# Kernel tuning notes

Measured on AMD Instinct MI355X. Metric: run time of the kernel, lower is better.

## Reference

```python
import jax, jax.numpy as jnp
import numpy as np

DIM, HEADS, DH, CHUNK, DEPTH = 1024, 8, 128, 64, 2
BATCH, SEQLEN = 2, 4096
MAX_LR = 0.01
EPS = 1e-6


def _rmsnorm(x, g=None):
    y = x * jax.lax.rsqrt(jnp.mean(x * x, axis=-1, keepdims=True) + EPS)
    return y * g if g is not None else y


def _mem_mlp(ws, x):
    # MemoryMLP: x @ W0, then silu before each subsequent layer
    x = x @ ws[0]
    for w in ws[1:]:
        x = jax.nn.silu(x) @ w
    return x


def _assoc_scan(gates, x):
    # y_t = gates_t * y_{t-1} + x_t along axis 3 (chunk axis)
    g = jnp.broadcast_to(gates, x.shape)
    def op(a, b):
        ga, xa = a
        gb, xb = b
        return ga * gb, gb * xa + xb
    _, y = jax.lax.associative_scan(op, (g, x), axis=3)
    return y


def setup_inputs() -> dict:
    key = jax.random.key(0)
    ks = jax.random.split(key, 12)
    b, n, d, h, dh = BATCH, SEQLEN, DIM, HEADS, DH
    di = h * dh
    lin = lambda k, i, o: jax.random.normal(k, (i, o), jnp.float32) * np.float32(1.0 / np.sqrt(i))
    return {
        "seq": jax.random.normal(ks[0], (b, n, d), jnp.float32),
        "store_norm_g": jnp.ones((d,), jnp.float32),
        "retrieve_norm_g": jnp.ones((d,), jnp.float32),
        "w_kv": lin(ks[1], d, 2 * di),
        "w_q": lin(ks[2], d, di),
        "w_step": lin(ks[3], d, h),
        "w_mom": lin(ks[4], d, h),
        "w_decay": lin(ks[5], d, h),
        "w_gate": lin(ks[6], d, h),
        "w_combine": lin(ks[7], di, d),
        "mh_gamma": jnp.zeros((h, 1, dh), jnp.float32),
        "mem_w0": lin(ks[8], dh, dh),
        "mem_w1": lin(ks[9], dh, dh),
    }


def reference(seq, store_norm_g, retrieve_norm_g, w_kv, w_q, w_step, w_mom,
              w_decay, w_gate, w_combine, mh_gamma, mem_w0, mem_w1):
    b, n, d = seq.shape
    h, dh, c = HEADS, DH, CHUNK
    nc = n // c
    mem_ws = (mem_w0, mem_w1)

    # ---------------- store memories (chunked test-time training) ----------------
    ss = _rmsnorm(seq, store_norm_g)                                    # (b,n,d)
    lr = jax.nn.sigmoid(jnp.einsum('bnd,dh->bhn', ss, w_step)) * MAX_LR  # adaptive step
    lr = lr.reshape(b, h, nc, c)
    cmean = ss.reshape(b, nc, c, d).mean(axis=2)                        # chunk mean-reduce
    mom_gate = jax.nn.sigmoid(jnp.einsum('bnd,dh->bhn', cmean, w_mom))   # (b,h,nc)
    decay = jax.nn.sigmoid(jnp.einsum('bnd,dh->bhn', cmean, w_decay))    # (b,h,nc)

    kv = ss @ w_kv                                                      # (b,n,2*h*dh)
    keys, values = jnp.split(kv, 2, axis=-1)
    split = lambda t: t.reshape(b, n, h, dh).transpose(0, 2, 1, 3).reshape(b, h, nc, c, dh)
    keys, values = split(keys), split(values)

    # per-chunk grad of weighted mse wrt memory MLP weights (vmap(grad), as in torch.func)
    def chunk_loss(ws, k, lrc, v):
        pred = _mem_mlp(ws, k)                                          # (c,dh)
        return jnp.sum(jnp.mean((pred - v) ** 2, axis=-1) * lrc)
    flat = lambda t: t.reshape(b * h * nc, c, dh)
    grads = jax.vmap(jax.grad(chunk_loss), in_axes=(None, 0, 0, 0))(
        mem_ws, flat(keys), lr.reshape(b * h * nc, c), flat(values))
    grads = jnp.stack([g.reshape(b, h, nc, dh, dh) for g in grads])     # (depth,b,h,nc,dh,dh)
    surprise = -grads

    gm = mom_gate[None, :, :, :, None, None]
    gd = (1.0 - decay)[None, :, :, :, None, None]
    momentum = _assoc_scan(gm, surprise)                                # momentum scan over chunks
    updates = _assoc_scan(gd, momentum)                                 # decayed cumulative weight deltas

    # ---------------- retrieve memories ----------------
    sr = _rmsnorm(seq, retrieve_norm_g)
    sr = jnp.pad(sr[:, c - 1:], ((0, 0), (0, c - 1), (0, 0)))           # causal shift by chunk-1
    q = (sr @ w_q).reshape(b, n, h, dh).transpose(0, 2, 1, 3).reshape(b, h, nc, c, dh)

    w0 = mem_w0 + updates[0]                                            # (b,h,nc,dh,dh)
    w1 = mem_w1 + updates[1]
    x = jnp.einsum('bhncd,bhnde->bhnce', q, w0)
    vals = jnp.einsum('bhncd,bhnde->bhnce', jax.nn.silu(x), w1)         # (b,h,nc,c,dh)
    vals = vals.reshape(b, h, n, dh)

    vals = _rmsnorm(vals) * (mh_gamma + 1.0)                            # multihead rmsnorm
    gate = jax.nn.sigmoid(jnp.einsum('bnd,dh->bhn', sr, w_gate))[..., None]
    vals = vals * gate                                                  # retrieve gate (heads>1)
    vals = vals.transpose(0, 2, 1, 3).reshape(b, n, h * dh)             # merge heads
    out = vals @ w_combine                                              # combine heads
    out = jnp.pad(out, ((0, 0), (c - 1, 0), (0, 0)))[:, :n]             # restore alignment
    return out
```

## Files before the change

### kernel.cpp

```cpp
#include <hip/hip_runtime.h>
#include <stdint.h>


#define SEQ 4096
#define NTOK 8192

typedef unsigned short u16;
typedef __attribute__((ext_vector_type(8))) short short8;
typedef __attribute__((ext_vector_type(4))) float f32x4;
typedef __attribute__((ext_vector_type(2))) unsigned int u32x2;

__device__ __forceinline__ u16 f2b(float f) {
  union { float f; uint32_t u; } c; c.f = f;
  uint32_t u = c.u;
  uint32_t r = (u + 0x7fffu + ((u >> 16) & 1u)) >> 16;
  return (u16)r;
}
__device__ __forceinline__ float b2f(u16 h) {
  union { uint32_t u; float f; } c; c.u = ((uint32_t)h) << 16;
  return c.f;
}
__device__ __forceinline__ float sigm(float x) { return 1.f / (1.f + __expf(-x)); }
__device__ __forceinline__ uint32_t pk2(float a, float b) {
  return (uint32_t)f2b(a) | ((uint32_t)f2b(b) << 16);
}
__device__ __forceinline__ void gl16(const void* g, void* l) {
  __builtin_amdgcn_global_load_lds(
      (const __attribute__((address_space(1))) unsigned int*)g,
      (__attribute__((address_space(3))) unsigned int*)l, 16, 0, 0);
}

__device__ __forceinline__ int sidx(int r, int c) {
  return r*128 + ((((c>>3) ^ (r&7))<<3) | (c&7));
}
__device__ __forceinline__ short8 frag_row_lds128(const u16* buf, int row, int ks, int l4) {
  int g = ks*4 + l4;
  return *(const short8*)&buf[row*128 + ((g ^ (row&7))<<3)];
}
__device__ __forceinline__ short8 frag_tile(const u16* t, int row, int ks, int l4) {
  return *(const short8*)&t[row*64 + (((ks*4 + l4) ^ (row&7))<<3)];
}
__device__ __forceinline__ int taddr(int c, int r0) {
  return c*64 + (r0 ^ ((c&7)<<3));
}


__global__ __launch_bounds__(256) void transpose_bf16(
    const float* __restrict__ src, u16* __restrict__ dst, int R, int C)
{
  __shared__ u16 tile[64*66];
  int tiles_x = C >> 6;
  int tx = blockIdx.x % tiles_x, ty = blockIdx.x / tiles_x;
  int c0 = tx*64, r0 = ty*64;
#pragma unroll
  for (int it=0; it<16; ++it) {
    int idx = it*256 + threadIdx.x;
    int rr = idx>>6, cc = idx&63;
    tile[cc*66 + rr] = f2b(src[(size_t)(r0+rr)*C + c0+cc]);
  }
  __syncthreads();
#pragma unroll
  for (int it=0; it<16; ++it) {
    int idx = it*256 + threadIdx.x;
    int rr = idx>>6, cc = idx&63;
    dst[(size_t)(c0+rr)*R + r0+cc] = tile[rr*66 + cc];
  }
}

__global__ __launch_bounds__(256) void smallprep(
    const float* __restrict__ w0, const float* __restrict__ w1,
    u16* __restrict__ w0Ts, u16* __restrict__ w1Ts, u16* __restrict__ w1bs)
{
  int id = blockIdx.x*256 + threadIdx.x;
  int i = id>>7, j = id&127;
  float a = w0[id], b = w1[id];
  w0Ts[sidx(j,i)] = f2b(a);
  w1Ts[sidx(j,i)] = f2b(b);
  w1bs[sidx(i,j)] = f2b(b);
}

__global__ __launch_bounds__(256) void proj_prep(
    const float* __restrict__ wstep, const float* __restrict__ wgatew,
    u16* __restrict__ Bt16)
{
  int id = blockIdx.x*256 + threadIdx.x;
  int n = id>>10, k = id&1023;
  float v = (n < 8) ? wstep[k*8 + n] : wgatew[k*8 + (n-8)];
  Bt16[id] = f2b(v);
}


__global__ __launch_bounds__(256) void norms_only(
    const float* __restrict__ seq, const float* __restrict__ gs,
    const float* __restrict__ gr, u16* __restrict__ ss, u16* __restrict__ sr)
{
  int w = threadIdx.x>>6, lane = threadIdx.x&63;
  int t = blockIdx.x*4 + w;
  const float* row = seq + (size_t)t*1024;
  f32x4 x[4];
  float ssq = 0.f;
#pragma unroll
  for (int j=0;j<4;++j) {
    x[j] = *(const f32x4*)&row[j*256 + lane*4];
    ssq += x[j][0]*x[j][0] + x[j][1]*x[j][1] + x[j][2]*x[j][2] + x[j][3]*x[j][3];
  }
  for (int m=32;m;m>>=1) ssq += __shfl_xor(ssq, m);
  float inv = rsqrtf(ssq*(1.f/1024.f) + 1e-6f);
#pragma unroll
  for (int j=0;j<4;++j) {
    int d = j*256 + lane*4;
    f32x4 g4 = *(const f32x4*)&gs[d];
    f32x4 r4 = *(const f32x4*)&gr[d];
    u32x2 ps, pr;
    ps[0] = pk2(x[j][0]*inv*g4[0], x[j][1]*inv*g4[1]);
    ps[1] = pk2(x[j][2]*inv*g4[2], x[j][3]*inv*g4[3]);
    pr[0] = pk2(x[j][0]*inv*r4[0], x[j][1]*inv*r4[1]);
    pr[1] = pk2(x[j][2]*inv*r4[2], x[j][3]*inv*r4[3]);
    *(u32x2*)&ss[(size_t)t*1024 + d] = ps;
    *(u32x2*)&sr[(size_t)t*1024 + d] = pr;
  }
}


__global__ __launch_bounds__(64) void proj_kernel(
    const u16* __restrict__ ss, const u16* __restrict__ sr,
    const u16* __restrict__ Bt16, float* __restrict__ lr,
    float* __restrict__ gate)
{
  int lane = threadIdx.x;
  int l15 = lane&15, l4 = lane>>4;
  size_t t0 = (size_t)blockIdx.x*16;
  f32x4 acc1 = {}, acc2 = {};
#pragma unroll 8
  for (int ks=0; ks<32; ++ks) {
    int kof = ks*32 + l4*8;
    short8 bf = *(const short8*)&Bt16[l15*1024 + kof];
    short8 as = *(const short8*)&ss[(t0+l15)*1024 + kof];
    short8 ar = *(const short8*)&sr[(t0+l15)*1024 + kof];
    acc1 = __builtin_amdgcn_mfma_f32_16x16x32_bf16(as, bf, acc1, 0,0,0);
    acc2 = __builtin_amdgcn_mfma_f32_16x16x32_bf16(ar, bf, acc2, 0,0,0);
  }
  int col = l15;
#pragma unroll
  for (int j=0;j<4;++j) {
    int t = (int)t0 + l4*4 + j;
    int b = t>>12, pos = t&4095;
    if (col < 8) lr[((size_t)(b*8+col))*4096 + pos] = sigm(acc1[j])*0.01f;
    else gate[((size_t)(b*8+(col-8)))*4096 + pos] = sigm(acc2[j]);
  }
}


__global__ __launch_bounds__(256) void chunkgates_kernel(
    const u16* __restrict__ ss, const float* __restrict__ wmom,
    const float* __restrict__ wdec, float* __restrict__ mg,
    float* __restrict__ d1m)
{
  int bc = blockIdx.x; int b = bc>>6, ch = bc&63;
  size_t t0 = (size_t)(b*4096 + ch*64)*1024;
  int tid = threadIdx.x;
  float cm[4]; cm[0]=cm[1]=cm[2]=cm[3]=0.f;
  for (int tok=0; tok<64; ++tok) {
#pragma unroll
    for (int i=0;i<4;++i)
      cm[i] += b2f(ss[t0 + (size_t)tok*1024 + i*256 + tid]);
  }
  float pm[8], pd[8];
#pragma unroll
  for (int h=0;h<8;++h){ pm[h]=0.f; pd[h]=0.f; }
#pragma unroll
  for (int i=0;i<4;++i) {
    float v = cm[i]*(1.f/64.f);
    int d = i*256+tid;
#pragma unroll
    for (int h=0;h<8;++h){ pm[h]+=v*wmom[d*8+h]; pd[h]+=v*wdec[d*8+h]; }
  }
#pragma unroll
  for (int h=0;h<8;++h)
    for (int m=32;m;m>>=1){ pm[h] += __shfl_xor(pm[h],m); pd[h] += __shfl_xor(pd[h],m); }
  __shared__ float r2[4][16];
  int wv = tid>>6;
  if ((tid&63)==0) {
#pragma unroll
    for (int h=0;h<8;++h){ r2[wv][h]=pm[h]; r2[wv][8+h]=pd[h]; }
  }
  __syncthreads();
  if (tid < 16) {
    float s = r2[0][tid]+r2[1][tid]+r2[2][tid]+r2[3][tid];
    if (tid<8) mg[(b*8+tid)*64 + ch] = sigm(s);
    else d1m[(b*8+(tid-8))*64 + ch] = 1.f - sigm(s);
  }
}


__global__ __launch_bounds__(512, 4) void gemm_bt(
    const u16* __restrict__ A, const u16* __restrict__ Bt,
    void* __restrict__ C, int M, int N, int K, int out_f32,
    u16* __restrict__ kvT)
{
  __shared__ __align__(16) u16 As[2][128*64];
  __shared__ __align__(16) u16 Bs[2][128*64];
  int tid = threadIdx.x;
  int w = tid>>6, lane = tid&63;
  int wr = w>>2, wc = w&3;
  int l15 = lane&15, l4 = lane>>4;
  int rl = lane>>3;
  int cg = (lane&7) ^ rl;
  int nwg = gridDim.x*gridDim.y;
  int wg  = blockIdx.y*gridDim.x + blockIdx.x;
  int cpx = nwg >> 3;
  int swz = (wg & 7)*cpx + (wg >> 3);
  int bx = swz % gridDim.x, by = swz / gridDim.x;
  int brow = by*128, bcol = bx*128;
  f32x4 acc[4][2] = {};

  auto STAGE = [&](int buf, int kt) {
#pragma unroll
    for (int i=0;i<2;++i) {
      int row = w*16 + i*8;
      gl16(&A [(size_t)(brow+row+rl)*K + kt + cg*8], &As[buf][row*64]);
      gl16(&Bt[(size_t)(bcol+row+rl)*K + kt + cg*8], &Bs[buf][row*64]);
    }
  };

  int nk = K >> 6;
  STAGE(0, 0);
  asm volatile("s_waitcnt vmcnt(0)");
  __syncthreads();
  for (int t=0; t<nk; ++t) {
    int cur = t & 1;
    if (t+1 < nk) STAGE(cur^1, (t+1)*64);
#pragma unroll
    for (int ks=0; ks<2; ++ks) {
      short8 af[4], bf[2];
#pragma unroll
      for (int m=0;m<4;++m) {
        int row = wr*64 + m*16 + l15;
        int g = ks*4 + l4;
        af[m] = *(const short8*)&As[cur][row*64 + ((g ^ (row&7))<<3)];
      }
#pragma unroll
      for (int n=0;n<2;++n) {
        int row = wc*32 + n*16 + l15;
        int g = ks*4 + l4;
        bf[n] = *(const short8*)&Bs[cur][row*64 + ((g ^ (row&7))<<3)];
      }
#pragma unroll
      for (int m=0;m<4;++m)
#pragma unroll
        for (int n=0;n<2;++n)
          acc[m][n] = __builtin_amdgcn_mfma_f32_16x16x32_bf16(af[m], bf[n], acc[m][n], 0,0,0);
    }
    asm volatile("s_waitcnt vmcnt(0)");
    __syncthreads();
  }
#pragma unroll
  for (int m=0;m<4;++m) {
#pragma unroll
    for (int n=0;n<2;++n) {
      int col = bcol + wc*32 + n*16 + l15;
#pragma unroll
      for (int j=0;j<4;++j) {
        int row = brow + wr*64 + m*16 + l4*4 + j;
        if (out_f32) ((float*)C)[(size_t)row*N + col] = acc[m][n][j];
        else ((u16*)C)[(size_t)row*N + col] = f2b(acc[m][n][j]);
      }
    }
  }
  if (kvT) {
#pragma unroll
    for (int m=0;m<4;++m) {
#pragma unroll
      for (int n=0;n<2;++n) {
        int col = bcol + wc*32 + n*16 + l15;
        if (col < 1024) {
          int row0 = brow + wr*64 + m*16 + l4*4;
          int d = col & 127;
          int chunk = ((row0>>12)*8 + (col>>7))*64 + ((row0&4095)>>6);
          int rr = row0 & 63;
          u32x2 p; p[0] = pk2(acc[m][n][0], acc[m][n][1]);
                   p[1] = pk2(acc[m][n][2], acc[m][n][3]);
          *(u32x2*)&kvT[(size_t)chunk*8192 + taddr(d, rr)] = p;
        }
      }
    }
  }
}


__global__ __launch_bounds__(512) void mlp_fwd(
    const u16* __restrict__ kvout, const float* __restrict__ lr,
    const u16* __restrict__ w0Ts, const u16* __restrict__ w1Ts,
    const u16* __restrict__ w1bs,
    u16* __restrict__ aTg, u16* __restrict__ dpTg, u16* __restrict__ dxTg)
{
  __shared__ __align__(16) u16 W0L[16384];
  __shared__ __align__(16) u16 W1L[16384];
  __shared__ __align__(16) u16 WBL[16384];
  __shared__ __align__(16) u16 abuf[16384];
  int tid = threadIdx.x;
  int w = tid>>6, lane = tid&63;
  int l15 = lane&15, l4 = lane>>4;
#pragma unroll
  for (int it=0; it<4; ++it) {
    int wb = it*512 + w*64;
    gl16((const short8*)w0Ts + wb + lane, (short8*)W0L + wb);
    gl16((const short8*)w1Ts + wb + lane, (short8*)W1L + wb);
    gl16((const short8*)w1bs + wb + lane, (short8*)WBL + wb);
  }
  __syncthreads();
  u16* ab = abuf + w*2048;
  int r0 = l4*4;
  int q = w&3, half = w>>2;
  int rb = q*16;
#pragma unroll
  for (int it2=0; it2<2; ++it2) {
    int cidx = blockIdx.x*4 + it2*2 + half;
    int bh = cidx>>6, ch = cidx&63;
    int b = bh>>3, hh = bh&7;
    size_t t0 = (size_t)(b*4096 + ch*64 + rb);
    size_t tout = (size_t)cidx*8192;
    f32x4 lrv = *(const f32x4*)&lr[(size_t)bh*4096 + ch*64 + rb + r0];

    f32x4 x1[8] = {};
#pragma unroll
    for (int ks=0; ks<4; ++ks) {
      short8 af = *(const short8*)&kvout[(t0 + l15)*2048 + hh*128 + ks*32 + l4*8];
#pragma unroll
      for (int n=0;n<8;++n) {
        short8 bf = frag_row_lds128(W0L, n*16+l15, ks, l4);
        x1[n] = __builtin_amdgcn_mfma_f32_16x16x32_bf16(af, bf, x1[n], 0,0,0);
      }
    }
#pragma unroll
    for (int n=0;n<8;++n) {
      int c = n*16 + l15;
      float av[4];
#pragma unroll
      for (int j=0;j<4;++j){ float xv = x1[n][j]; av[j] = xv*sigm(xv); }
      ab[sidx(r0+0,c)] = f2b(av[0]);
      ab[sidx(r0+1,c)] = f2b(av[1]);
      ab[sidx(r0+2,c)] = f2b(av[2]);
      ab[sidx(r0+3,c)] = f2b(av[3]);
      u32x2 p; p[0] = pk2(av[0],av[1]); p[1] = pk2(av[2],av[3]);
      *(u32x2*)&aTg[tout + taddr(c, rb + r0)] = p;
    }
    f32x4 pr[8] = {};
#pragma unroll
    for (int ks=0; ks<4; ++ks) {
      short8 af = frag_row_lds128(ab, l15, ks, l4);
#pragma unroll
      for (int n=0;n<8;++n) {
        short8 bf = frag_row_lds128(W1L, n*16+l15, ks, l4);
        pr[n] = __builtin_amdgcn_mfma_f32_16x16x32_bf16(af, bf, pr[n], 0,0,0);
      }
    }
#pragma unroll
    for (int n=0;n<8;++n) {
      int c = n*16 + l15;
      float dv[4];
#pragma unroll
      for (int j=0;j<4;++j) {
        float vv = b2f(kvout[(t0+r0+j)*2048 + 1024 + hh*128 + c]);
        dv[j] = 0.015625f * lrv[j] * (pr[n][j] - vv);
      }
      ab[sidx(r0+0,c)] = f2b(dv[0]);
      ab[sidx(r0+1,c)] = f2b(dv[1]);
      ab[sidx(r0+2,c)] = f2b(dv[2]);
      ab[sidx(r0+3,c)] = f2b(dv[3]);
      u32x2 p; p[0] = pk2(dv[0],dv[1]); p[1] = pk2(dv[2],dv[3]);
      *(u32x2*)&dpTg[tout + taddr(c, rb + r0)] = p;
    }
    f32x4 da[8] = {};
#pragma unroll
    for (int ks=0; ks<4; ++ks) {
      short8 af = frag_row_lds128(ab, l15, ks, l4);
#pragma unroll
      for (int n=0;n<8;++n) {
        short8 bf = frag_row_lds128(WBL, n*16+l15, ks, l4);
        da[n] = __builtin_amdgcn_mfma_f32_16x16x32_bf16(af, bf, da[n], 0,0,0);
      }
    }
#pragma unroll
    for (int n=0;n<8;++n) {
      int c = n*16 + l15;
      float d[4];
#pragma unroll
      for (int j=0;j<4;++j) {
        float xv = x1[n][j];
        float sg = sigm(xv);
        d[j] = da[n][j]*(sg*(1.f + xv*(1.f - sg)));
      }
      u32x2 p; p[0] = pk2(d[0],d[1]); p[1] = pk2(d[2],d[3]);
      *(u32x2*)&dxTg[tout + taddr(c, rb + r0)] = p;
    }
  }
}


__global__ __launch_bounds__(256) void grad_op(
    const u16* __restrict__ dpT, const u16* __restrict__ aT,
    const u16* __restrict__ dxT, const u16* __restrict__ kT,
    u16* __restrict__ S)
{
  __shared__ __align__(16) u16 lds[16384];
  int bid = blockIdx.x;
  int op = bid >> 10;
  int sub = bid & 1023, bh = sub>>6, ch = sub&63;
  size_t tin = (size_t)sub*8192;
  const u16* Ain = op ? (dxT + tin) : (dpT + tin);
  const u16* Bin = op ? (kT  + tin) : (aT  + tin);
  int tid = threadIdx.x;
  int w = tid>>6, lane = tid&63;
  int l15 = lane&15, l4 = lane>>4;

#pragma unroll
  for (int it=0; it<4; ++it) {
    int wb = it*256 + w*64;
    gl16((const short8*)Ain + wb + lane, (short8*)lds + wb);
    gl16((const short8*)Bin + wb + lane, (short8*)(lds+8192) + wb);
  }
  __syncthreads();

  f32x4 g[2][8] = {};
#pragma unroll
  for (int ks=0; ks<2; ++ks) {
    short8 af[2];
#pragma unroll
    for (int mi=0; mi<2; ++mi)
      af[mi] = frag_tile(lds, w*32 + mi*16 + l15, ks, l4);
#pragma unroll
    for (int n=0;n<8;++n) {
      short8 bf = frag_tile(lds+8192, n*16 + l15, ks, l4);
#pragma unroll
      for (int mi=0;mi<2;++mi)
        g[mi][n] = __builtin_amdgcn_mfma_f32_16x16x32_bf16(af[mi], bf, g[mi][n], 0,0,0);
    }
  }
  __syncthreads();

#pragma unroll
  for (int mi=0;mi<2;++mi)
#pragma unroll
    for (int n=0;n<8;++n)
#pragma unroll
      for (int j=0;j<4;++j) {
        int m = w*32 + mi*16 + l4*4 + j, c = n*16 + l15;
        lds[sidx(m,c)] = f2b(-g[mi][n][j]);
      }
  __syncthreads();

  u16* Sout = S + ((size_t)((op ? bh : 16+bh))*64 + ch)*16384;
#pragma unroll
  for (int it=0; it<8; ++it)
    ((short8*)Sout)[it*256+tid] = ((const short8*)lds)[it*256+tid];
}


__global__ __launch_bounds__(256) void scan_kernel(
    u16* __restrict__ S, const float* __restrict__ mg, const float* __restrict__ d1m,
    const u16* __restrict__ w0Ts, const u16* __restrict__ w1Ts)
{
  int bidx = blockIdx.x;
  int eblk = bidx & 31;
  int mbh = bidx >> 5;
  int bh = mbh & 15;
  int e = (eblk*256 + threadIdx.x)*2;
  uint32_t* base = (uint32_t*)(S + (size_t)mbh*64*16384 + e);
  const u16* wsrc = (mbh < 16) ? w0Ts : w1Ts;
  uint32_t wp = *(const uint32_t*)&wsrc[e];
  float wv0 = b2f((u16)(wp & 0xffffu)), wv1 = b2f((u16)(wp >> 16));
  const float* g1 = mg + bh*64;
  const float* g2 = d1m + bh*64;
  float mom0=0.f, upd0=0.f, mom1=0.f, upd1=0.f;
  for (int c2=0; c2<64; ++c2) {
    uint32_t s2 = base[(size_t)c2*8192];
    float s0 = b2f((u16)(s2 & 0xffffu)), s1 = b2f((u16)(s2 >> 16));
    float gg1 = g1[c2], gg2 = g2[c2];
    mom0 = gg1*mom0 + s0; upd0 = gg2*upd0 + mom0;
    mom1 = gg1*mom1 + s1; upd1 = gg2*upd1 + mom1;
    base[(size_t)c2*8192] = pk2(wv0 + upd0, wv1 + upd1);
  }
}


__global__ __launch_bounds__(256) void retrieve_kernel(
    const u16* __restrict__ qn, const u16* __restrict__ W,
    const float* __restrict__ gamma, const float* __restrict__ gate,
    u16* __restrict__ vals)
{
  __shared__ __align__(16) u16 W0s[16384];
  __shared__ __align__(16) u16 W1s[16384];
  __shared__ __align__(16) u16 QA[8192];
  int bid = blockIdx.x;
  int bh = bid>>6, ch = bid&63;
  int b = bh>>3, h = bh&7;
  int tid = threadIdx.x;
  int w = tid>>6, lane = tid&63;
  int l15 = lane&15, l4 = lane>>4;
  const u16* W0g = W + ((size_t)bh*64 + ch)*16384;
  const u16* W1g = W + ((size_t)(16+bh)*64 + ch)*16384;
#pragma unroll
  for (int it=0; it<8; ++it) {
    int wb = it*256 + w*64;
    gl16((const short8*)W0g + wb + lane, (short8*)W0s + wb);
    gl16((const short8*)W1g + wb + lane, (short8*)W1s + wb);
  }
  u16* qa = QA + w*2048;
#pragma unroll
  for (int it=0; it<4; ++it) {
    int task = it*64 + lane;
    int rloc = task>>4, g = task&15;
    int posn = ch*64 + w*16 + rloc + 63;
    short8 v;
    if (posn < 4096) v = *(const short8*)&qn[((size_t)(b*4096+posn))*1024 + h*128 + g*8];
    else {
#pragma unroll
      for (int i=0;i<8;++i) v[i]=0;
    }
    *(short8*)&qa[rloc*128 + ((g ^ (rloc&7))<<3)] = v;
  }
  __syncthreads();
  f32x4 xx[8] = {};
#pragma unroll
  for (int ks=0; ks<4; ++ks) {
    short8 af = frag_row_lds128(qa, l15, ks, l4);
#pragma unroll
    for (int n=0;n<8;++n) {
      short8 bf = frag_row_lds128(W0s, n*16+l15, ks, l4);
      xx[n] = __builtin_amdgcn_mfma_f32_16x16x32_bf16(af, bf, xx[n], 0,0,0);
    }
  }
  int r0 = l4*4;
#pragma unroll
  for (int n=0;n<8;++n) {
    int c = n*16 + l15;
#pragma unroll
    for (int j=0;j<4;++j) {
      float xv = xx[n][j];
      qa[sidx(r0+j,c)] = f2b(xv * sigm(xv));
    }
  }
  f32x4 vv[8] = {};
#pragma unroll
  for (int ks=0; ks<4; ++ks) {
    short8 af = frag_row_lds128(qa, l15, ks, l4);
#pragma unroll
    for (int n=0;n<8;++n) {
      short8 bf = frag_row_lds128(W1s, n*16+l15, ks, l4);
      vv[n] = __builtin_amdgcn_mfma_f32_16x16x32_bf16(af, bf, vv[n], 0,0,0);
    }
  }
#pragma unroll
  for (int j=0;j<4;++j) {
    float ssq = 0.f;
#pragma unroll
    for (int n=0;n<8;++n) ssq += vv[n][j]*vv[n][j];
    ssq += __shfl_xor(ssq,1); ssq += __shfl_xor(ssq,2);
    ssq += __shfl_xor(ssq,4); ssq += __shfl_xor(ssq,8);
    float rms = rsqrtf(ssq*(1.f/128.f) + 1e-6f);
    int posn = ch*64 + w*16 + r0 + j + 63;
    if (posn < 4096) {
      float gt = gate[(size_t)bh*4096 + posn];
      size_t orow = ((size_t)(b*4096+posn))*1024 + h*128;
#pragma unroll
      for (int n=0;n<8;++n) {
        int c = n*16 + l15;
        vals[orow + c] = f2b(vv[n][j]*rms*(1.f + gamma[h*128+c])*gt);
      }
    }
  }
}

extern "C" void kernel_launch(void* const* d_in, const int* in_sizes, int n_in,
                              void* d_out, int out_size, void* d_ws, size_t ws_size,
                              hipStream_t stream) {
  const float* seq    = (const float*)d_in[0];
  const float* gstore = (const float*)d_in[1];
  const float* gret   = (const float*)d_in[2];
  const float* wkv    = (const float*)d_in[3];
  const float* wq     = (const float*)d_in[4];
  const float* wstep  = (const float*)d_in[5];
  const float* wmom   = (const float*)d_in[6];
  const float* wdec   = (const float*)d_in[7];
  const float* wgatew = (const float*)d_in[8];
  const float* wcomb  = (const float*)d_in[9];
  const float* gamma  = (const float*)d_in[10];
  const float* w0f    = (const float*)d_in[11];
  const float* w1f    = (const float*)d_in[12];
  float* out = (float*)d_out;
  (void)in_sizes; (void)n_in; (void)out_size; (void)ws_size;

  char* p = (char*)d_ws;
  size_t off = 0;
  auto alloc = [&](size_t bytes) -> void* {
    void* r = p + off; off += (bytes + 255) & ~(size_t)255; return r;
  };
  u16* wkvT   = (u16*)alloc((size_t)2048*1024*2);
  u16* wqT    = (u16*)alloc((size_t)1024*1024*2);
  u16* wcombT = (u16*)alloc((size_t)1024*1024*2);
  u16* w0Ts   = (u16*)alloc(16384*2);
  u16* w1Ts   = (u16*)alloc(16384*2);
  u16* w1bs   = (u16*)alloc(16384*2);
  u16* Bt16   = (u16*)alloc(16384*2);
  u16* ss     = (u16*)alloc((size_t)NTOK*1024*2);
  u16* sr     = (u16*)alloc((size_t)NTOK*1024*2);
  u16* kvout  = (u16*)alloc((size_t)NTOK*2048*2);
  u16* qn     = (u16*)alloc((size_t)NTOK*1024*2);
  u16* vals   = (u16*)alloc((size_t)NTOK*1024*2);
  float* lr   = (float*)alloc((size_t)16*4096*4);
  float* gate = (float*)alloc((size_t)16*4096*4);
  float* mg   = (float*)alloc(1024*4);
  float* d1m  = (float*)alloc(1024*4);
  u16* S      = (u16*)alloc((size_t)32*64*16384*2);
  u16* kTg    = (u16*)alloc((size_t)1024*8192*2);
  u16* aTg    = (u16*)alloc((size_t)1024*8192*2);
  u16* dpTg   = (u16*)alloc((size_t)1024*8192*2);
  u16* dxTg   = (u16*)alloc((size_t)1024*8192*2);

  transpose_bf16<<<dim3(512),dim3(256),0,stream>>>(wkv, wkvT, 1024, 2048);
  transpose_bf16<<<dim3(256),dim3(256),0,stream>>>(wq, wqT, 1024, 1024);
  transpose_bf16<<<dim3(256),dim3(256),0,stream>>>(wcomb, wcombT, 1024, 1024);
  smallprep<<<dim3(64),dim3(256),0,stream>>>(w0f, w1f, w0Ts, w1Ts, w1bs);
  proj_prep<<<dim3(64),dim3(256),0,stream>>>(wstep, wgatew, Bt16);
  norms_only<<<dim3(2048),dim3(256),0,stream>>>(seq, gstore, gret, ss, sr);
  proj_kernel<<<dim3(512),dim3(64),0,stream>>>(ss, sr, Bt16, lr, gate);
  chunkgates_kernel<<<dim3(128),dim3(256),0,stream>>>(ss, wmom, wdec, mg, d1m);
  gemm_bt<<<dim3(16,64),dim3(512),0,stream>>>(ss, wkvT, kvout, 8192, 2048, 1024, 0, kTg);
  gemm_bt<<<dim3(8,64),dim3(512),0,stream>>>(sr, wqT, qn, 8192, 1024, 1024, 0, nullptr);
  mlp_fwd<<<dim3(256),dim3(512),0,stream>>>(kvout, lr, w0Ts, w1Ts, w1bs, aTg, dpTg, dxTg);
  grad_op<<<dim3(2048),dim3(256),0,stream>>>(dpTg, aTg, dxTg, kTg, S);
  scan_kernel<<<dim3(1024),dim3(256),0,stream>>>(S, mg, d1m, w0Ts, w1Ts);
  hipMemsetAsync(vals, 0, 63*1024*2, stream);
  hipMemsetAsync(vals + (size_t)4096*1024, 0, 63*1024*2, stream);
  retrieve_kernel<<<dim3(1024),dim3(256),0,stream>>>(qn, S, gamma, gate, vals);
  gemm_bt<<<dim3(8,64),dim3(512),0,stream>>>(vals, wcombT, out, 8192, 1024, 1024, 1, nullptr);
}
```

Measured before the change: 238.3 us.

## Fuse per-chunk weight-gradient outer products into the MLP forward kernel

```diff
diff --git a/kernel.cpp b/kernel.cpp
--- a/kernel.cpp
+++ b/kernel.cpp
@@ -37,11 +37,15 @@
   int g = ks*4 + l4;
   return *(const short8*)&buf[row*128 + ((g ^ (row&7))<<3)];
 }
-__device__ __forceinline__ short8 frag_tile(const u16* t, int row, int ks, int l4) {
-  return *(const short8*)&t[row*64 + (((ks*4 + l4) ^ (row&7))<<3)];
-}
-__device__ __forceinline__ int taddr(int c, int r0) {
-  return c*64 + (r0 ^ ((c&7)<<3));
+__device__ __forceinline__ int swzOP(int dim, int k) {
+  return dim*32 + ((((k>>3) ^ (dim&3)))<<3) + (k&7);
+}
+__device__ __forceinline__ void opw4(u16* tb, int dim, int k0, uint32_t p0, uint32_t p1) {
+  u32x2 v; v[0] = p0; v[1] = p1;
+  *(u32x2*)&tb[swzOP(dim, k0)] = v;
+}
+__device__ __forceinline__ short8 opfrag(const u16* tb, int dim, int l4) {
+  return *(const short8*)&tb[dim*32 + ((l4 ^ (dim&3))<<3)];
 }
 
 
@@ -159,11 +163,14 @@
   int bc = blockIdx.x; int b = bc>>6, ch = bc&63;
   size_t t0 = (size_t)(b*4096 + ch*64)*1024;
   int tid = threadIdx.x;
+  int d0 = tid*4;
   float cm[4]; cm[0]=cm[1]=cm[2]=cm[3]=0.f;
   for (int tok=0; tok<64; ++tok) {
-#pragma unroll
-    for (int i=0;i<4;++i)
-      cm[i] += b2f(ss[t0 + (size_t)tok*1024 + i*256 + tid]);
+    u32x2 v2 = *(const u32x2*)&ss[t0 + (size_t)tok*1024 + d0];
+    cm[0] += b2f((u16)(v2[0] & 0xffffu));
+    cm[1] += b2f((u16)(v2[0] >> 16));
+    cm[2] += b2f((u16)(v2[1] & 0xffffu));
+    cm[3] += b2f((u16)(v2[1] >> 16));
   }
   float pm[8], pd[8];
 #pragma unroll
@@ -171,7 +178,7 @@
 #pragma unroll
   for (int i=0;i<4;++i) {
     float v = cm[i]*(1.f/64.f);
-    int d = i*256+tid;
+    int d = d0 + i;
 #pragma unroll
     for (int h=0;h<8;++h){ pm[h]+=v*wmom[d*8+h]; pd[h]+=v*wdec[d*8+h]; }
   }
@@ -278,9 +285,10 @@
           int d = col & 127;
           int chunk = ((row0>>12)*8 + (col>>7))*64 + ((row0&4095)>>6);
           int rr = row0 & 63;
+          int hf = rr >> 5, r5 = rr & 31;
           u32x2 p; p[0] = pk2(acc[m][n][0], acc[m][n][1]);
                    p[1] = pk2(acc[m][n][2], acc[m][n][3]);
-          *(u32x2*)&kvT[(size_t)chunk*8192 + taddr(d, rr)] = p;
+          *(u32x2*)&kvT[(size_t)chunk*8192 + hf*4096 + swzOP(d, r5)] = p;
         }
       }
     }
@@ -288,11 +296,11 @@
 }
 
 
-__global__ __launch_bounds__(512) void mlp_fwd(
+__global__ __launch_bounds__(512) void mlp_grad(
     const u16* __restrict__ kvout, const float* __restrict__ lr,
     const u16* __restrict__ w0Ts, const u16* __restrict__ w1Ts,
-    const u16* __restrict__ w1bs,
-    u16* __restrict__ aTg, u16* __restrict__ dpTg, u16* __restrict__ dxTg)
+    const u16* __restrict__ w1bs, const u16* __restrict__ kTg,
+    u16* __restrict__ S)
 {
   __shared__ __align__(16) u16 W0L[16384];
   __shared__ __align__(16) u16 W1L[16384];
@@ -311,15 +319,16 @@
   __syncthreads();
   u16* ab = abuf + w*2048;
   int r0 = l4*4;
-  int q = w&3, half = w>>2;
-  int rb = q*16;
-#pragma unroll
+  int q4 = w&3, half = w>>2;
+  int rb = q4*16;
+  int k0 = (q4&1)*16 + r0;
+  u16* ob = abuf + half*8192;
+
   for (int it2=0; it2<2; ++it2) {
     int cidx = blockIdx.x*4 + it2*2 + half;
     int bh = cidx>>6, ch = cidx&63;
     int b = bh>>3, hh = bh&7;
     size_t t0 = (size_t)(b*4096 + ch*64 + rb);
-    size_t tout = (size_t)cidx*8192;
     f32x4 lrv = *(const f32x4*)&lr[(size_t)bh*4096 + ch*64 + rb + r0];
 
     f32x4 x1[8] = {};
@@ -332,6 +341,7 @@
         x1[n] = __builtin_amdgcn_mfma_f32_16x16x32_bf16(af, bf, x1[n], 0,0,0);
       }
     }
+    uint32_t a_pk[16];
 #pragma unroll
     for (int n=0;n<8;++n) {
       int c = n*16 + l15;
@@ -342,8 +352,8 @@
       ab[sidx(r0+1,c)] = f2b(av[1]);
       ab[sidx(r0+2,c)] = f2b(av[2]);
       ab[sidx(r0+3,c)] = f2b(av[3]);
-      u32x2 p; p[0] = pk2(av[0],av[1]); p[1] = pk2(av[2],av[3]);
-      *(u32x2*)&aTg[tout + taddr(c, rb + r0)] = p;
+      a_pk[n*2]   = pk2(av[0],av[1]);
+      a_pk[n*2+1] = pk2(av[2],av[3]);
     }
     f32x4 pr[8] = {};
 #pragma unroll
@@ -355,6 +365,7 @@
         pr[n] = __builtin_amdgcn_mfma_f32_16x16x32_bf16(af, bf, pr[n], 0,0,0);
       }
     }
+    uint32_t dp_pk[16];
 #pragma unroll
     for (int n=0;n<8;++n) {
       int c = n*16 + l15;
@@ -368,8 +379,8 @@
       ab[sidx(r0+1,c)] = f2b(dv[1]);
       ab[sidx(r0+2,c)] = f2b(dv[2]);
       ab[sidx(r0+3,c)] = f2b(dv[3]);
-      u32x2 p; p[0] = pk2(dv[0],dv[1]); p[1] = pk2(dv[2],dv[3]);
-      *(u32x2*)&dpTg[tout + taddr(c, rb + r0)] = p;
+      dp_pk[n*2]   = pk2(dv[0],dv[1]);
+      dp_pk[n*2+1] = pk2(dv[2],dv[3]);
     }
     f32x4 da[8] = {};
 #pragma unroll
@@ -381,9 +392,9 @@
         da[n] = __builtin_amdgcn_mfma_f32_16x16x32_bf16(af, bf, da[n], 0,0,0);
       }
     }
+    uint32_t dx_pk[16];
 #pragma unroll
     for (int n=0;n<8;++n) {
-      int c = n*16 + l15;
       float d[4];
 #pragma unroll
       for (int j=0;j<4;++j) {
@@ -391,69 +402,85 @@
         float sg = sigm(xv);
         d[j] = da[n][j]*(sg*(1.f + xv*(1.f - sg)));
       }
-      u32x2 p; p[0] = pk2(d[0],d[1]); p[1] = pk2(d[2],d[3]);
-      *(u32x2*)&dxTg[tout + taddr(c, rb + r0)] = p;
-    }
-  }
-}
-
-
-__global__ __launch_bounds__(256) void grad_op(
-    const u16* __restrict__ dpT, const u16* __restrict__ aT,
-    const u16* __restrict__ dxT, const u16* __restrict__ kT,
-    u16* __restrict__ S)
-{
-  __shared__ __align__(16) u16 lds[16384];
-  int bid = blockIdx.x;
-  int op = bid >> 10;
-  int sub = bid & 1023, bh = sub>>6, ch = sub&63;
-  size_t tin = (size_t)sub*8192;
-  const u16* Ain = op ? (dxT + tin) : (dpT + tin);
-  const u16* Bin = op ? (kT  + tin) : (aT  + tin);
-  int tid = threadIdx.x;
-  int w = tid>>6, lane = tid&63;
-  int l15 = lane&15, l4 = lane>>4;
-
-#pragma unroll
-  for (int it=0; it<4; ++it) {
-    int wb = it*256 + w*64;
-    gl16((const short8*)Ain + wb + lane, (short8*)lds + wb);
-    gl16((const short8*)Bin + wb + lane, (short8*)(lds+8192) + wb);
-  }
-  __syncthreads();
-
-  f32x4 g[2][8] = {};
-#pragma unroll
-  for (int ks=0; ks<2; ++ks) {
-    short8 af[2];
-#pragma unroll
-    for (int mi=0; mi<2; ++mi)
-      af[mi] = frag_tile(lds, w*32 + mi*16 + l15, ks, l4);
-#pragma unroll
-    for (int n=0;n<8;++n) {
-      short8 bf = frag_tile(lds+8192, n*16 + l15, ks, l4);
+      dx_pk[n*2]   = pk2(d[0],d[1]);
+      dx_pk[n*2+1] = pk2(d[2],d[3]);
+    }
+
+    f32x4 g1[2][8] = {};
+#pragma unroll
+    for (int hf=0; hf<2; ++hf) {
+      __syncthreads();
+      if ((q4>>1) == hf) {
+#pragma unroll
+        for (int n=0;n<8;++n) {
+          int c = n*16 + l15;
+          opw4(ob,      c, k0, dp_pk[n*2], dp_pk[n*2+1]);
+          opw4(ob+4096, c, k0, a_pk[n*2],  a_pk[n*2+1]);
+        }
+      }
+      __syncthreads();
+#pragma unroll
+      for (int n=0;n<8;++n) {
+        short8 bf = opfrag(ob+4096, n*16 + l15, l4);
+#pragma unroll
+        for (int mi=0;mi<2;++mi) {
+          short8 af = opfrag(ob, q4*32 + mi*16 + l15, l4);
+          g1[mi][n] = __builtin_amdgcn_mfma_f32_16x16x32_bf16(af, bf, g1[mi][n], 0,0,0);
+        }
+      }
+    }
+    {
+      u16* S1 = S + ((size_t)(16+bh)*64 + ch)*16384;
 #pragma unroll
       for (int mi=0;mi<2;++mi)
-        g[mi][n] = __builtin_amdgcn_mfma_f32_16x16x32_bf16(af[mi], bf, g[mi][n], 0,0,0);
-    }
-  }
-  __syncthreads();
-
-#pragma unroll
-  for (int mi=0;mi<2;++mi)
-#pragma unroll
-    for (int n=0;n<8;++n)
-#pragma unroll
-      for (int j=0;j<4;++j) {
-        int m = w*32 + mi*16 + l4*4 + j, c = n*16 + l15;
-        lds[sidx(m,c)] = f2b(-g[mi][n][j]);
-      }
-  __syncthreads();
-
-  u16* Sout = S + ((size_t)((op ? bh : 16+bh))*64 + ch)*16384;
-#pragma unroll
-  for (int it=0; it<8; ++it)
-    ((short8*)Sout)[it*256+tid] = ((const short8*)lds)[it*256+tid];
+#pragma unroll
+        for (int n=0;n<8;++n)
+#pragma unroll
+          for (int j=0;j<4;++j) {
+            int m = q4*32 + mi*16 + l4*4 + j, c = n*16 + l15;
+            S1[sidx(m,c)] = f2b(-g1[mi][n][j]);
+          }
+    }
+    f32x4 g0[2][8] = {};
+    const u16* kts = kTg + (size_t)cidx*8192;
+#pragma unroll
+    for (int hf=0; hf<2; ++hf) {
+      __syncthreads();
+      if ((q4>>1) == hf) {
+#pragma unroll
+        for (int n=0;n<8;++n)
+          opw4(ob, n*16 + l15, k0, dx_pk[n*2], dx_pk[n*2+1]);
+      }
+#pragma unroll
+      for (int it=0; it<2; ++it) {
+        int off = it*2048 + q4*512;
+        gl16(kts + hf*4096 + off + lane*8, ob + 4096 + off);
+      }
+      __syncthreads();
+#pragma unroll
+      for (int n=0;n<8;++n) {
+        short8 bf = opfrag(ob+4096, n*16 + l15, l4);
+#pragma unroll
+        for (int mi=0;mi<2;++mi) {
+          short8 af = opfrag(ob, q4*32 + mi*16 + l15, l4);
+          g0[mi][n] = __builtin_amdgcn_mfma_f32_16x16x32_bf16(af, bf, g0[mi][n], 0,0,0);
+        }
+      }
+    }
+    {
+      u16* S0 = S + ((size_t)bh*64 + ch)*16384;
+#pragma unroll
+      for (int mi=0;mi<2;++mi)
+#pragma unroll
+        for (int n=0;n<8;++n)
+#pragma unroll
+          for (int j=0;j<4;++j) {
+            int m = q4*32 + mi*16 + l4*4 + j, c = n*16 + l15;
+            S0[sidx(m,c)] = f2b(-g0[mi][n][j]);
+          }
+    }
+    __syncthreads();
+  }
 }
 
 
@@ -614,9 +641,6 @@
   float* d1m  = (float*)alloc(1024*4);
   u16* S      = (u16*)alloc((size_t)32*64*16384*2);
   u16* kTg    = (u16*)alloc((size_t)1024*8192*2);
-  u16* aTg    = (u16*)alloc((size_t)1024*8192*2);
-  u16* dpTg   = (u16*)alloc((size_t)1024*8192*2);
-  u16* dxTg   = (u16*)alloc((size_t)1024*8192*2);
 
   transpose_bf16<<<dim3(512),dim3(256),0,stream>>>(wkv, wkvT, 1024, 2048);
   transpose_bf16<<<dim3(256),dim3(256),0,stream>>>(wq, wqT, 1024, 1024);
@@ -628,8 +652,7 @@
   chunkgates_kernel<<<dim3(128),dim3(256),0,stream>>>(ss, wmom, wdec, mg, d1m);
   gemm_bt<<<dim3(16,64),dim3(512),0,stream>>>(ss, wkvT, kvout, 8192, 2048, 1024, 0, kTg);
   gemm_bt<<<dim3(8,64),dim3(512),0,stream>>>(sr, wqT, qn, 8192, 1024, 1024, 0, nullptr);
-  mlp_fwd<<<dim3(256),dim3(512),0,stream>>>(kvout, lr, w0Ts, w1Ts, w1bs, aTg, dpTg, dxTg);
-  grad_op<<<dim3(2048),dim3(256),0,stream>>>(dpTg, aTg, dxTg, kTg, S);
+  mlp_grad<<<dim3(256),dim3(512),0,stream>>>(kvout, lr, w0Ts, w1Ts, w1bs, kTg, S);
   scan_kernel<<<dim3(1024),dim3(256),0,stream>>>(S, mg, d1m, w0Ts, w1Ts);
   hipMemsetAsync(vals, 0, 63*1024*2, stream);
   hipMemsetAsync(vals + (size_t)4096*1024, 0, 63*1024*2, stream);
```

Result: slower. 307.9 us (+29.2%).
